# Kernel optimization log

Hardware: AMD Instinct MI355X
Metric: run time of the kernel (lower is better)

The kernel has to match this reference:

```python
import jax, jax.numpy as jnp
import numpy as np

KERAS_EPSILON = 1e-7  # keras.backend.epsilon()


def setup_inputs() -> dict:
    key = jax.random.key(0)
    x = jax.random.normal(key, (4, 2048, 128), dtype=jnp.float32)
    return {"x": x}


def reference(x) -> jnp.ndarray:
    # Euclidean distance matrix: D[b, i, j] = sqrt(sum_d (x[b,i,d] - x[b,j,d])^2 + eps)
    # Computed via the ||a||^2 + ||b||^2 - 2 a.b identity to avoid the
    # [B, N, N, D] broadcasted intermediate of the original implementation.
    sq = jnp.sum(x * x, axis=-1)                      # [B, N]
    cross = jnp.einsum("bnd,bmd->bnm", x, x)           # [B, N, N]
    d2 = sq[:, :, None] + sq[:, None, :] - 2.0 * cross  # [B, N, N]
    d2 = jnp.maximum(d2, 0.0)  # clamp tiny negative rounding errors
    return jnp.sqrt(d2 + KERAS_EPSILON)
```

## Files before the change

### kernel.cpp

```cpp
#include <hip/hip_runtime.h>
#include <hip/hip_bf16.h>

typedef __attribute__((ext_vector_type(8))) __bf16 bf16x8;
typedef __attribute__((ext_vector_type(4))) float  f32x4;

constexpr int NN   = 2048;
constexpr int DD   = 128;
constexpr int TI   = 128;
constexpr int TJ   = 64;
constexpr int LDSS = 136;

__global__ __launch_bounds__(256, 2)
void edm_kernel(const float* __restrict__ x, float* __restrict__ out) {
    __shared__ __align__(16) __bf16 As[TI * LDSS];
    __shared__ __align__(16) __bf16 Bs[TJ * LDSS];
    __shared__ float sqA[TI];
    __shared__ float sqB[TJ];

    const int t  = threadIdx.x;
    const int jt = blockIdx.x;
    const int it = blockIdx.y;
    const int b  = blockIdx.z;

    const float* xb = x + (size_t)b * NN * DD;

    {
        const float* src = xb + (size_t)it * TI * DD;
        #pragma unroll
        for (int iter = 0; iter < 8; ++iter) {
            const int idx = t + iter * 256;
            const int row = idx >> 4;
            const int c16 = idx & 15;
            const float4* p = (const float4*)(src + row * DD + c16 * 8);
            const float4 v0 = p[0];
            const float4 v1 = p[1];
            bf16x8 w;
            w[0] = (__bf16)v0.x; w[1] = (__bf16)v0.y;
            w[2] = (__bf16)v0.z; w[3] = (__bf16)v0.w;
            w[4] = (__bf16)v1.x; w[5] = (__bf16)v1.y;
            w[6] = (__bf16)v1.z; w[7] = (__bf16)v1.w;
            *(bf16x8*)&As[row * LDSS + c16 * 8] = w;
        }
        const float* srcB = xb + (size_t)jt * TJ * DD;
        #pragma unroll
        for (int iter = 0; iter < 4; ++iter) {
            const int idx = t + iter * 256;
            const int row = idx >> 4;
            const int c16 = idx & 15;
            const float4* p = (const float4*)(srcB + row * DD + c16 * 8);
            const float4 v0 = p[0];
            const float4 v1 = p[1];
            bf16x8 w;
            w[0] = (__bf16)v0.x; w[1] = (__bf16)v0.y;
            w[2] = (__bf16)v0.z; w[3] = (__bf16)v0.w;
            w[4] = (__bf16)v1.x; w[5] = (__bf16)v1.y;
            w[6] = (__bf16)v1.z; w[7] = (__bf16)v1.w;
            *(bf16x8*)&Bs[row * LDSS + c16 * 8] = w;
        }
    }
    __syncthreads();

    if (t < TI + TJ) {
        const __bf16* r = (t < TI) ? &As[t * LDSS] : &Bs[(t - TI) * LDSS];
        float s = 0.f;
        #pragma unroll
        for (int k = 0; k < DD; k += 8) {
            bf16x8 v = *(const bf16x8*)(r + k);
            #pragma unroll
            for (int j = 0; j < 8; ++j) { const float f = (float)v[j]; s += f * f; }
        }
        if (t < TI) sqA[t] = s; else sqB[t - TI] = s;
    }
    __syncthreads();

    const int wave = t >> 6;
    const int lane = t & 63;
    const int wm = (wave >> 1) * 64;
    const int wn = (wave & 1) * 32;
    const int lm = lane & 15;
    const int q  = lane >> 4;

    f32x4 acc[4][2] = {};
    #pragma unroll
    for (int ks = 0; ks < 4; ++ks) {
        const int kb = ks * 32 + q * 8;
        bf16x8 a[4], bb[2];
        #pragma unroll
        for (int mf = 0; mf < 4; ++mf)
            a[mf] = *(const bf16x8*)&As[(wm + mf * 16 + lm) * LDSS + kb];
        #pragma unroll
        for (int nf = 0; nf < 2; ++nf)
            bb[nf] = *(const bf16x8*)&Bs[(wn + nf * 16 + lm) * LDSS + kb];
        #pragma unroll
        for (int mf = 0; mf < 4; ++mf)
            #pragma unroll
            for (int nf = 0; nf < 2; ++nf)
                acc[mf][nf] = __builtin_amdgcn_mfma_f32_16x16x32_bf16(
                    a[mf], bb[nf], acc[mf][nf], 0, 0, 0);
    }

    float* outp = out + ((size_t)b * NN + (size_t)it * TI) * NN + (size_t)jt * TJ;
    #pragma unroll
    for (int mf = 0; mf < 4; ++mf) {
        #pragma unroll
        for (int nf = 0; nf < 2; ++nf) {
            const int col = wn + nf * 16 + lm;
            const float sj = sqB[col];
            #pragma unroll
            for (int r = 0; r < 4; ++r) {
                const int row = wm + mf * 16 + q * 4 + r;
                float d2 = sqA[row] + sj - 2.0f * acc[mf][nf][r];
                d2 = fmaxf(d2, 0.0f);
                outp[(size_t)row * NN + col] = sqrtf(d2 + 1e-7f);
            }
        }
    }
}

extern "C" void kernel_launch(void* const* d_in, const int* in_sizes, int n_in,
                              void* d_out, int out_size, void* d_ws, size_t ws_size,
                              hipStream_t stream) {
    const float* x = (const float*)d_in[0];
    float* out = (float*)d_out;
    dim3 grid(NN / TJ, NN / TI, 4);
    edm_kernel<<<grid, dim3(256), 0, stream>>>(x, out);
}
```

Measured before the change: 85.83 us.

## Precompute bf16 swizzled inputs and norms, use direct global-to-LDS loads and vectorized stores

```diff
diff --git a/kernel.cpp b/kernel.cpp
--- a/kernel.cpp
+++ b/kernel.cpp
@@ -8,70 +8,70 @@
 constexpr int DD   = 128;
 constexpr int TI   = 128;
 constexpr int TJ   = 64;
-constexpr int LDSS = 136;
+constexpr int ROWB = 256;
 
-__global__ __launch_bounds__(256, 2)
-void edm_kernel(const float* __restrict__ x, float* __restrict__ out) {
-    __shared__ __align__(16) __bf16 As[TI * LDSS];
-    __shared__ __align__(16) __bf16 Bs[TJ * LDSS];
-    __shared__ float sqA[TI];
-    __shared__ float sqB[TJ];
+__device__ __forceinline__ void gload_lds16(const void* g, void* l) {
+    __builtin_amdgcn_global_load_lds(
+        (const __attribute__((address_space(1))) void*)g,
+        (__attribute__((address_space(3))) void*)l, 16, 0, 0);
+}
+
+__global__ __launch_bounds__(256)
+void edm_prep(const float* __restrict__ x, __bf16* __restrict__ xb,
+              float* __restrict__ sq) {
+    const int t  = threadIdx.x;
+    const int rl = t >> 4;
+    const int c  = t & 15;
+    const int g  = blockIdx.x * 16 + rl;
+
+    const float4* p = (const float4*)(x + (size_t)g * DD + c * 8);
+    const float4 v0 = p[0];
+    const float4 v1 = p[1];
+    bf16x8 w;
+    w[0] = (__bf16)v0.x; w[1] = (__bf16)v0.y;
+    w[2] = (__bf16)v0.z; w[3] = (__bf16)v0.w;
+    w[4] = (__bf16)v1.x; w[5] = (__bf16)v1.y;
+    w[6] = (__bf16)v1.z; w[7] = (__bf16)v1.w;
+
+    float s = 0.f;
+    #pragma unroll
+    for (int j = 0; j < 8; ++j) { const float f = (float)w[j]; s += f * f; }
+
+    const int byte = (c * 16) ^ ((g & 7) << 4);
+    *(bf16x8*)((char*)xb + (size_t)g * ROWB + byte) = w;
+
+    s += __shfl_xor(s, 1);
+    s += __shfl_xor(s, 2);
+    s += __shfl_xor(s, 4);
+    s += __shfl_xor(s, 8);
+    if (c == 0) sq[g] = s;
+}
+
+__global__ __launch_bounds__(256, 3)
+void edm_main(const __bf16* __restrict__ xb, const float* __restrict__ sq,
+              float* __restrict__ out) {
+    __shared__ __align__(16) char As[TI * ROWB];
+    __shared__ __align__(16) char Bs[TJ * ROWB];
 
     const int t  = threadIdx.x;
     const int jt = blockIdx.x;
     const int it = blockIdx.y;
     const int b  = blockIdx.z;
 
-    const float* xb = x + (size_t)b * NN * DD;
+    const char* xbase = (const char*)xb + (size_t)b * NN * ROWB;
+    const char* srcA  = xbase + (size_t)it * TI * ROWB;
+    const char* srcB  = xbase + (size_t)jt * TJ * ROWB;
 
-    {
-        const float* src = xb + (size_t)it * TI * DD;
-        #pragma unroll
-        for (int iter = 0; iter < 8; ++iter) {
-            const int idx = t + iter * 256;
-            const int row = idx >> 4;
-            const int c16 = idx & 15;
-            const float4* p = (const float4*)(src + row * DD + c16 * 8);
-            const float4 v0 = p[0];
-            const float4 v1 = p[1];
-            bf16x8 w;
-            w[0] = (__bf16)v0.x; w[1] = (__bf16)v0.y;
-            w[2] = (__bf16)v0.z; w[3] = (__bf16)v0.w;
-            w[4] = (__bf16)v1.x; w[5] = (__bf16)v1.y;
-            w[6] = (__bf16)v1.z; w[7] = (__bf16)v1.w;
-            *(bf16x8*)&As[row * LDSS + c16 * 8] = w;
-        }
-        const float* srcB = xb + (size_t)jt * TJ * DD;
-        #pragma unroll
-        for (int iter = 0; iter < 4; ++iter) {
-            const int idx = t + iter * 256;
-            const int row = idx >> 4;
-            const int c16 = idx & 15;
-            const float4* p = (const float4*)(srcB + row * DD + c16 * 8);
-            const float4 v0 = p[0];
-            const float4 v1 = p[1];
-            bf16x8 w;
-            w[0] = (__bf16)v0.x; w[1] = (__bf16)v0.y;
-            w[2] = (__bf16)v0.z; w[3] = (__bf16)v0.w;
-            w[4] = (__bf16)v1.x; w[5] = (__bf16)v1.y;
-            w[6] = (__bf16)v1.z; w[7] = (__bf16)v1.w;
-            *(bf16x8*)&Bs[row * LDSS + c16 * 8] = w;
-        }
+    #pragma unroll
+    for (int i = 0; i < 8; ++i) {
+        const int off = (t + i * 256) * 16;
+        gload_lds16(srcA + off, As + off);
     }
-    __syncthreads();
-
-    if (t < TI + TJ) {
-        const __bf16* r = (t < TI) ? &As[t * LDSS] : &Bs[(t - TI) * LDSS];
-        float s = 0.f;
-        #pragma unroll
-        for (int k = 0; k < DD; k += 8) {
-            bf16x8 v = *(const bf16x8*)(r + k);
-            #pragma unroll
-            for (int j = 0; j < 8; ++j) { const float f = (float)v[j]; s += f * f; }
-        }
-        if (t < TI) sqA[t] = s; else sqB[t - TI] = s;
+    #pragma unroll
+    for (int i = 0; i < 4; ++i) {
+        const int off = (t + i * 256) * 16;
+        gload_lds16(srcB + off, Bs + off);
     }
-    __syncthreads();
 
     const int wave = t >> 6;
     const int lane = t & 63;
@@ -79,40 +79,59 @@
     const int wn = (wave & 1) * 32;
     const int lm = lane & 15;
     const int q  = lane >> 4;
+    const int swz = (lm & 7) << 4;
+
+    const float* sqi = sq + b * NN + it * TI;
+    const float* sqj = sq + b * NN + jt * TJ;
+    float si[4];
+    #pragma unroll
+    for (int mf = 0; mf < 4; ++mf) si[mf] = sqi[wm + mf * 16 + lm];
+    f32x4 sj[2];
+    #pragma unroll
+    for (int nf = 0; nf < 2; ++nf)
+        sj[nf] = *(const f32x4*)(sqj + wn + nf * 16 + q * 4);
+
+    __syncthreads();
 
     f32x4 acc[4][2] = {};
     #pragma unroll
     for (int ks = 0; ks < 4; ++ks) {
-        const int kb = ks * 32 + q * 8;
+        const int cb = ks * 64 + q * 16;
         bf16x8 a[4], bb[2];
         #pragma unroll
-        for (int mf = 0; mf < 4; ++mf)
-            a[mf] = *(const bf16x8*)&As[(wm + mf * 16 + lm) * LDSS + kb];
+        for (int mf = 0; mf < 4; ++mf) {
+            const int row = wm + mf * 16 + lm;
+            a[mf] = *(const bf16x8*)(As + row * ROWB + (cb ^ swz));
+        }
         #pragma unroll
-        for (int nf = 0; nf < 2; ++nf)
-            bb[nf] = *(const bf16x8*)&Bs[(wn + nf * 16 + lm) * LDSS + kb];
+        for (int nf = 0; nf < 2; ++nf) {
+            const int row = wn + nf * 16 + lm;
+            bb[nf] = *(const bf16x8*)(Bs + row * ROWB + (cb ^ swz));
+        }
         #pragma unroll
         for (int mf = 0; mf < 4; ++mf)
             #pragma unroll
             for (int nf = 0; nf < 2; ++nf)
                 acc[mf][nf] = __builtin_amdgcn_mfma_f32_16x16x32_bf16(
-                    a[mf], bb[nf], acc[mf][nf], 0, 0, 0);
+                    bb[nf], a[mf], acc[mf][nf], 0, 0, 0);
     }
 
     float* outp = out + ((size_t)b * NN + (size_t)it * TI) * NN + (size_t)jt * TJ;
     #pragma unroll
     for (int mf = 0; mf < 4; ++mf) {
+        const int i = wm + mf * 16 + lm;
+        float* rowp = outp + (size_t)i * NN;
+        const float base = si[mf];
         #pragma unroll
         for (int nf = 0; nf < 2; ++nf) {
-            const int col = wn + nf * 16 + lm;
-            const float sj = sqB[col];
+            f32x4 d;
             #pragma unroll
             for (int r = 0; r < 4; ++r) {
-                const int row = wm + mf * 16 + q * 4 + r;
-                float d2 = sqA[row] + sj - 2.0f * acc[mf][nf][r];
+                float d2 = base + sj[nf][r] - 2.0f * acc[mf][nf][r];
                 d2 = fmaxf(d2, 0.0f);
-                outp[(size_t)row * NN + col] = sqrtf(d2 + 1e-7f);
+                d[r] = sqrtf(d2 + 1e-7f);
             }
+            *(f32x4*)(rowp + wn + nf * 16 + q * 4) = d;
         }
     }
 }
@@ -122,6 +141,8 @@
                               hipStream_t stream) {
     const float* x = (const float*)d_in[0];
     float* out = (float*)d_out;
-    dim3 grid(NN / TJ, NN / TI, 4);
-    edm_kernel<<<grid, dim3(256), 0, stream>>>(x, out);
+    float*  sqw = (float*)d_ws;
+    __bf16* xbw = (__bf16*)((char*)d_ws + 32768);
+    edm_prep<<<dim3((4 * NN) / 16), dim3(256), 0, stream>>>(x, xbw, sqw);
+    edm_main<<<dim3(NN / TJ, NN / TI, 4), dim3(256), 0, stream>>>(xbw, sqw, out);
 }
```

Result: no change. 85.15 us (-0.8%).
